# Performance work log

Hardware: AMD Instinct MI355X
Metric: run time of the kernel (lower is better)

## Reference

```python
import jax, jax.numpy as jnp
import numpy as np

NUM_HEADS = 12
ROPE_THETA = 10000.0


def _rope_cos_sin(n, hd, dtype):
    inv_freq = 1.0 / (ROPE_THETA ** (np.arange(0, hd, 2, dtype=np.float64) / hd))
    freqs = np.outer(np.arange(n, dtype=np.float64), inv_freq)  # (N, hd/2)
    emb = np.concatenate([freqs, freqs], axis=-1)               # (N, hd)
    return jnp.asarray(np.cos(emb), dtype), jnp.asarray(np.sin(emb), dtype)


def _apply_rope(t, cos, sin):
    # t: (B, H, N, hd); rotate-half convention
    half = t.shape[-1] // 2
    t1, t2 = t[..., :half], t[..., half:]
    rot = jnp.concatenate([-t2, t1], axis=-1)
    return t * cos + rot * sin


def setup_inputs() -> dict:
    key = jax.random.key(0)
    k1, k2, k3 = jax.random.split(key, 3)
    B, N, C = 8, 1024, 768
    x = jax.random.normal(k1, (B, N, C), dtype=jnp.float32)
    w_qkv = jax.random.normal(k2, (C, 3 * C), dtype=jnp.float32) * 0.02
    w_proj = jax.random.normal(k3, (C, C), dtype=jnp.float32) * 0.02
    b_proj = jnp.zeros((C,), dtype=jnp.float32)
    return {"x": x, "w_qkv": w_qkv, "w_proj": w_proj, "b_proj": b_proj}


def reference(x, w_qkv, w_proj, b_proj):
    B, N, C = x.shape
    H = NUM_HEADS
    hd = C // H
    scale = hd ** -0.5
    # qkv: (B,N,3C) -> (B,N,3,H,hd) -> (B,H,3,N,hd)
    qkv = (x @ w_qkv).reshape(B, N, 3, H, hd).transpose(0, 3, 2, 1, 4)
    q, k, v = qkv[:, :, 0], qkv[:, :, 1], qkv[:, :, 2]  # each (B,H,N,hd)
    cos, sin = _rope_cos_sin(N, hd, x.dtype)
    q = _apply_rope(q, cos, sin)
    k = _apply_rope(k, cos, sin)
    attn = jax.nn.softmax(jnp.einsum("bhqd,bhkd->bhqk", q, k) * scale, axis=-1)
    out = jnp.einsum("bhqk,bhkd->bhqd", attn, v)  # (B,H,N,hd)
    out = out.transpose(0, 2, 1, 3).reshape(B, N, C)
    return out @ w_proj + b_proj
```

## Files before the change

kernel.cpp:

```cpp
#include <hip/hip_runtime.h>

typedef unsigned short ushort_t;
typedef __bf16 bf16x8 __attribute__((ext_vector_type(8)));
typedef float f32x4 __attribute__((ext_vector_type(4)));
typedef unsigned short u16x8 __attribute__((ext_vector_type(8)));
typedef unsigned int u32x2 __attribute__((ext_vector_type(2)));

#define MFMA16(a, b, c) __builtin_amdgcn_mfma_f32_16x16x32_bf16((a), (b), (c), 0, 0, 0)

#define SEQ 1024
#define NHEAD 12
#define HD 64
#define CDIM 768
#define TS 6291456
#define QSCALE 0.1803368801111204f

__device__ __forceinline__ ushort_t f2bf(float f) {
  __bf16 b = (__bf16)f;
  return __builtin_bit_cast(ushort_t, b);
}
__device__ __forceinline__ unsigned pk2(float lo, float hi) {
  return (unsigned)f2bf(lo) | ((unsigned)f2bf(hi) << 16);
}

typedef __attribute__((address_space(1))) void gvoid_t;
typedef __attribute__((address_space(3))) void lvoid_t;
__device__ __forceinline__ void async16(const ushort_t* g, ushort_t* l) {
  __builtin_amdgcn_global_load_lds((gvoid_t*)g, (lvoid_t*)l, 16, 0, 0);
}

__device__ __forceinline__ void transpose_body(const float* __restrict__ in,
                                               ushort_t* __restrict__ out,
                                               int R, int C, int bxi, int byi,
                                               float (*tile)[33]) {
  int bx = bxi * 32, by = byi * 32;
  int tx = threadIdx.x & 31, ty = threadIdx.x >> 5;
#pragma unroll
  for (int i = ty; i < 32; i += 8) {
    int r = by + i, c = bx + tx;
    if (r < R && c < C) tile[i][tx] = in[(size_t)r * C + c];
  }
  __syncthreads();
#pragma unroll
  for (int i = ty; i < 32; i += 8) {
    int r = bx + i, c = by + tx;
    if (r < C && c < R) out[(size_t)r * R + c] = f2bf(tile[tx][i]);
  }
}

__global__ void __launch_bounds__(256) prep_all(const float* __restrict__ x,
                                                const float* __restrict__ w_qkv,
                                                const float* __restrict__ w_proj,
                                                ushort_t* __restrict__ xb,
                                                ushort_t* __restrict__ wqkvT,
                                                ushort_t* __restrict__ wprojT,
                                                float* __restrict__ tab) {
  __shared__ float tile[32][33];
  const int bid = blockIdx.x;
  if (bid < 3072) {
    int i = (bid * 256 + threadIdx.x) * 8;
    float4 a = *(const float4*)(x + i);
    float4 b = *(const float4*)(x + i + 4);
    u16x8 r;
    r[0] = f2bf(a.x); r[1] = f2bf(a.y); r[2] = f2bf(a.z); r[3] = f2bf(a.w);
    r[4] = f2bf(b.x); r[5] = f2bf(b.y); r[6] = f2bf(b.z); r[7] = f2bf(b.w);
    *(u16x8*)(xb + i) = r;
  } else if (bid < 3072 + 1728) {
    int t = bid - 3072;
    transpose_body(w_qkv, wqkvT, 768, 2304, t % 72, t / 72, tile);
  } else if (bid < 3072 + 1728 + 576) {
    int t = bid - (3072 + 1728);
    transpose_body(w_proj, wprojT, 768, 768, t % 24, t / 24, tile);
  } else {
    int g = (bid - 5376) * 256 + threadIdx.x;
    int n = g >> 5, j = g & 31;
    double invf = pow(10000.0, -((double)(2 * j)) / 64.0);
    double fr = (double)n * invf;
    tab[g * 2]     = (float)cos(fr);
    tab[g * 2 + 1] = (float)sin(fr);
  }
}

__device__ __forceinline__ void gemm_bt_core(const ushort_t* __restrict__ A,
                                             const ushort_t* __restrict__ Bt,
                                             int K, int bm, int bn,
                                             ushort_t (*ldsA)[4096],
                                             ushort_t (*ldsB)[4096],
                                             f32x4 acc[4][4]) {
  const int tid = threadIdx.x;
  const int lane = tid & 63, wid = tid >> 6;
  const int wm = (wid >> 1) * 64, wn = (wid & 1) * 64;
  const int fr = lane & 15, fq = lane >> 4;
#pragma unroll
  for (int i = 0; i < 4; ++i)
#pragma unroll
    for (int j = 0; j < 4; ++j) acc[i][j] = (f32x4){0.f, 0.f, 0.f, 0.f};

  const int srow = tid >> 2;
  const int scol = (tid & 3) * 8;
  const size_t aOff = (size_t)(bm + srow) * K + scol;
  const size_t bOff = (size_t)(bn + srow) * K + scol;
  const int nIter = K >> 6;

  for (int kt = 0; kt < nIter; ++kt) {
    const int k0 = kt * 64;
#pragma unroll
    for (int h = 0; h < 2; ++h) {
      async16(A + aOff + k0 + h * 32, ldsA[h] + tid * 8);
      async16(A + aOff + (size_t)64 * K + k0 + h * 32, ldsA[h] + 2048 + tid * 8);
      async16(Bt + bOff + k0 + h * 32, ldsB[h] + tid * 8);
      async16(Bt + bOff + (size_t)64 * K + k0 + h * 32, ldsB[h] + 2048 + tid * 8);
    }
    __syncthreads();
#pragma unroll
    for (int ks = 0; ks < 2; ++ks) {
      bf16x8 aF[4], bF[4];
#pragma unroll
      for (int i = 0; i < 4; ++i)
        aF[i] = *(const bf16x8*)(ldsA[ks] + (wm + i * 16 + fr) * 32 + fq * 8);
#pragma unroll
      for (int j = 0; j < 4; ++j)
        bF[j] = *(const bf16x8*)(ldsB[ks] + (wn + j * 16 + fr) * 32 + fq * 8);
#pragma unroll
      for (int i = 0; i < 4; ++i)
#pragma unroll
        for (int j = 0; j < 4; ++j) acc[i][j] = MFMA16(aF[i], bF[j], acc[i][j]);
    }
    __syncthreads();
  }
}

__global__ void __launch_bounds__(256) gemm_qkv(const ushort_t* __restrict__ A,
                                                const ushort_t* __restrict__ Bt,
                                                const float* __restrict__ tab,
                                                ushort_t* __restrict__ qkv) {
  __shared__ __attribute__((aligned(16))) ushort_t ldsA[2][4096];
  __shared__ __attribute__((aligned(16))) ushort_t ldsB[2][4096];
  f32x4 acc[4][4];
  const int f = blockIdx.x;
  const int xcd = f & 7, r = f >> 3;
  const int bm = (xcd * 8 + (r & 7)) * 128;
  const int bn = (r >> 3) * 128;
  gemm_bt_core(A, Bt, CDIM, bm, bn, ldsA, ldsB, acc);
  const int lane = threadIdx.x & 63, wid = threadIdx.x >> 6;
  const int wm = (wid >> 1) * 64, wn = (wid & 1) * 64;
  const int fr = lane & 15, fq = lane >> 4;
  const int tensor = bn / 768;

  if (tensor < 2) {
    ushort_t* dstT = qkv + (size_t)tensor * TS;
    const float qs = (tensor == 0) ? QSCALE : 1.0f;
#pragma unroll
    for (int i = 0; i < 4; ++i) {
#pragma unroll
      for (int jp = 0; jp < 2; ++jp) {
        const int col = bn + wn + jp * 16 + fr;
        const int rem = col - tensor * 768;
        const int h = rem >> 6;
        const int d2 = rem & 31;
#pragma unroll
        for (int rr = 0; rr < 4; ++rr) {
          const int row = bm + wm + i * 16 + fq * 4 + rr;
          const int b = row >> 10, n = row & 1023;
          const float2 cs = ((const float2*)tab)[n * 32 + d2];
          const float av = acc[i][jp][rr], bv = acc[i][jp + 2][rr];
          const float o1 = (av * cs.x - bv * cs.y) * qs;
          const float o2 = (bv * cs.x + av * cs.y) * qs;
          ushort_t* dst = dstT + ((size_t)(b * NHEAD + h) * SEQ + n) * HD + d2;
          dst[0]  = f2bf(o1);
          dst[32] = f2bf(o2);
        }
      }
    }
  } else {
    ushort_t* vt = qkv + 2 * (size_t)TS;
#pragma unroll
    for (int i = 0; i < 4; ++i) {
      const int row0 = bm + wm + i * 16 + fq * 4;
      const int b = row0 >> 10, n0 = row0 & 1023;
#pragma unroll
      for (int j = 0; j < 4; ++j) {
        const int col = bn + wn + j * 16 + fr;
        const int rem = col - 1536;
        const int h = rem >> 6, d = rem & 63;
        u32x2 pk;
        pk[0] = pk2(acc[i][j][0], acc[i][j][1]);
        pk[1] = pk2(acc[i][j][2], acc[i][j][3]);
        *(u32x2*)(vt + ((size_t)(b * NHEAD + h) * HD + d) * SEQ + n0) = pk;
      }
    }
  }
}

__global__ void __launch_bounds__(256) gemm_proj(const ushort_t* __restrict__ A,
                                                 const ushort_t* __restrict__ Bt,
                                                 const float* __restrict__ bias,
                                                 float* __restrict__ Cout) {
  __shared__ __attribute__((aligned(16))) ushort_t ldsA[2][4096];
  __shared__ __attribute__((aligned(16))) ushort_t ldsB[2][4096];
  f32x4 acc[4][4];
  const int f = blockIdx.x;
  const int xcd = f & 7, r = f >> 3;
  const int bm = (xcd * 8 + (r & 7)) * 128;
  const int bn = (r >> 3) * 128;
  gemm_bt_core(A, Bt, CDIM, bm, bn, ldsA, ldsB, acc);
  const int lane = threadIdx.x & 63, wid = threadIdx.x >> 6;
  const int wm = (wid >> 1) * 64, wn = (wid & 1) * 64;
  const int fr = lane & 15, fq = lane >> 4;
#pragma unroll
  for (int i = 0; i < 4; ++i) {
#pragma unroll
    for (int j = 0; j < 4; ++j) {
      const int col = bn + wn + j * 16 + fr;
      const float bv = bias[col];
#pragma unroll
      for (int rr = 0; rr < 4; ++rr) {
        const int row = bm + wm + i * 16 + fq * 4 + rr;
        Cout[(size_t)row * CDIM + col] = acc[i][j][rr] + bv;
      }
    }
  }
}

__global__ void __launch_bounds__(256, 3) attn_fused(const ushort_t* __restrict__ Qb,
                                                     const ushort_t* __restrict__ Kb,
                                                     const ushort_t* __restrict__ VTb,
                                                     ushort_t* __restrict__ Ob) {
  __shared__ __attribute__((aligned(16))) ushort_t ldsK[2][2][2048];
  __shared__ __attribute__((aligned(16))) ushort_t ldsV[2][2][2048];
  __shared__ __attribute__((aligned(16))) ushort_t Pl[4][32 * 72];

  const int tid = threadIdx.x, lane = tid & 63, wid = tid >> 6;
  const int fr = lane & 15, fq = lane >> 4;

  const int f = blockIdx.x;
  const int xp = f & 7, rest = f >> 3;
  const int g = rest % 12, qb = rest / 12;
  const int head = g * 8 + xp;
  const int q0 = qb * 128;

  const ushort_t* Qh  = Qb  + (size_t)head * (SEQ * HD);
  const ushort_t* Kh  = Kb  + (size_t)head * (SEQ * HD);
  const ushort_t* VTh = VTb + (size_t)head * (HD * SEQ);

  bf16x8 qF[2][2];
#pragma unroll
  for (int qt = 0; qt < 2; ++qt) {
    const int qrow = q0 + wid * 32 + qt * 16 + fr;
    qF[qt][0] = *(const bf16x8*)(Qh + (size_t)qrow * HD + fq * 8);
    qF[qt][1] = *(const bf16x8*)(Qh + (size_t)qrow * HD + 32 + fq * 8);
  }

  f32x4 ot[2][4];
#pragma unroll
  for (int qt = 0; qt < 2; ++qt)
#pragma unroll
    for (int dt = 0; dt < 4; ++dt) ot[qt][dt] = (f32x4){0.f, 0.f, 0.f, 0.f};
  float lsum[2] = {0.f, 0.f};

  const int srow = tid >> 2;
  const int sc = (tid & 3) * 8;

#define STAGE(buf, kt)                                                          \
  {                                                                             \
    const ushort_t* ksrc = Kh + (size_t)((kt) * 64 + srow) * HD + sc;           \
    async16(ksrc,      &ldsK[buf][0][tid * 8]);                                 \
    async16(ksrc + 32, &ldsK[buf][1][tid * 8]);                                 \
    const ushort_t* vsrc = VTh + (size_t)srow * SEQ + (kt) * 64 + sc;           \
    async16(vsrc,      &ldsV[buf][0][tid * 8]);                                 \
    async16(vsrc + 32, &ldsV[buf][1][tid * 8]);                                 \
  }

  STAGE(0, 0);
  __syncthreads();

  for (int kt = 0; kt < 16; ++kt) {
    const int cur = kt & 1;
    if (kt < 15) STAGE(cur ^ 1, kt + 1);

    bf16x8 kf[4][2];
#pragma unroll
    for (int t = 0; t < 4; ++t)
#pragma unroll
      for (int ks = 0; ks < 2; ++ks)
        kf[t][ks] = *(const bf16x8*)&ldsK[cur][ks][(t * 16 + fr) * 32 + fq * 8];

    f32x4 st[2][4];
#pragma unroll
    for (int qt = 0; qt < 2; ++qt)
#pragma unroll
      for (int t = 0; t < 4; ++t) {
        f32x4 s = (f32x4){0.f, 0.f, 0.f, 0.f};
        s = MFMA16(kf[t][0], qF[qt][0], s);
        s = MFMA16(kf[t][1], qF[qt][1], s);
        st[qt][t] = s;
      }

    bf16x8 vf[4][2];
#pragma unroll
    for (int dt = 0; dt < 4; ++dt)
#pragma unroll
      for (int ks = 0; ks < 2; ++ks)
        vf[dt][ks] = *(const bf16x8*)&ldsV[cur][ks][(dt * 16 + fr) * 32 + fq * 8];

#pragma unroll
    for (int qt = 0; qt < 2; ++qt) {
      ushort_t* Pw = &Pl[wid][(qt * 16 + fr) * 72];
      float ls = lsum[qt];
#pragma unroll
      for (int t = 0; t < 4; ++t) {
        const float e0 = exp2f(st[qt][t][0]);
        const float e1 = exp2f(st[qt][t][1]);
        const float e2 = exp2f(st[qt][t][2]);
        const float e3 = exp2f(st[qt][t][3]);
        ls += (e0 + e1) + (e2 + e3);
        u32x2 pk;
        pk[0] = pk2(e0, e1);
        pk[1] = pk2(e2, e3);
        *(u32x2*)(Pw + t * 16 + fq * 4) = pk;
      }
      lsum[qt] = ls;
      bf16x8 pf0 = *(const bf16x8*)(Pw + fq * 8);
      bf16x8 pf1 = *(const bf16x8*)(Pw + 32 + fq * 8);
#pragma unroll
      for (int dt = 0; dt < 4; ++dt) {
        ot[qt][dt] = MFMA16(vf[dt][0], pf0, ot[qt][dt]);
        ot[qt][dt] = MFMA16(vf[dt][1], pf1, ot[qt][dt]);
      }
    }
    __syncthreads();
  }

  const int b = head / NHEAD, h = head - b * NHEAD;
#pragma unroll
  for (int qt = 0; qt < 2; ++qt) {
    float l = lsum[qt];
    l += __shfl_xor(l, 16);
    l += __shfl_xor(l, 32);
    const float inv = 1.0f / l;
    const int qrow = q0 + wid * 32 + qt * 16 + fr;
    ushort_t* obase = Ob + ((size_t)(b * SEQ + qrow)) * CDIM + h * HD;
#pragma unroll
    for (int dt = 0; dt < 4; ++dt) {
      u32x2 pk;
      pk[0] = pk2(ot[qt][dt][0] * inv, ot[qt][dt][1] * inv);
      pk[1] = pk2(ot[qt][dt][2] * inv, ot[qt][dt][3] * inv);
      *(u32x2*)(obase + dt * 16 + fq * 4) = pk;
    }
  }
}

extern "C" void kernel_launch(void* const* d_in, const int* in_sizes, int n_in,
                              void* d_out, int out_size, void* d_ws, size_t ws_size,
                              hipStream_t stream) {
  const float* x      = (const float*)d_in[0];
  const float* w_qkv  = (const float*)d_in[1];
  const float* w_proj = (const float*)d_in[2];
  const float* b_proj = (const float*)d_in[3];
  float* out = (float*)d_out;
  char* ws = (char*)d_ws;

  ushort_t* xb     = (ushort_t*)(ws + 0);
  ushort_t* wqkvT  = (ushort_t*)(ws + 12582912);
  ushort_t* wprojT = (ushort_t*)(ws + 16121856);
  ushort_t* qkv    = (ushort_t*)(ws + 17301504);
  float*    tab    = (float*)  (ws + 55050240);
  ushort_t* oattn  = (ushort_t*)(ws + 55312384);

  prep_all<<<5504, 256, 0, stream>>>(x, w_qkv, w_proj, xb, wqkvT, wprojT, tab);
  gemm_qkv<<<1152, 256, 0, stream>>>(xb, wqkvT, tab, qkv);
  attn_fused<<<768, 256, 0, stream>>>(qkv, qkv + TS, qkv + 2 * (size_t)TS, oattn);
  gemm_proj<<<384, 256, 0, stream>>>(oattn, wprojT, b_proj, out);
}
```

Before: 210.9 us.

## Switch attention to 32x32x16 MFMA with register-resident P and swizzled LDS

Rewrites the attention kernel to use 32x32x16 bf16 MFMA tiles instead of 16x16x32, so each wave handles its 32 query rows with one accumulator per output half. The probability matrix is now rearranged into the B-operand layout with cross-half-wave shuffles instead of a round trip through a per-wave LDS buffer. K/V tiles are stored in LDS with an XOR-style swizzle to avoid bank conflicts. The aim is to cut LDS traffic and instruction count per tile. The cost is larger accumulator registers, and the occupancy hint in launch bounds is dropped.

```diff
diff --git a/kernel.cpp b/kernel.cpp
--- a/kernel.cpp
+++ b/kernel.cpp
@@ -3,10 +3,13 @@
 typedef unsigned short ushort_t;
 typedef __bf16 bf16x8 __attribute__((ext_vector_type(8)));
 typedef float f32x4 __attribute__((ext_vector_type(4)));
+typedef float f32x16 __attribute__((ext_vector_type(16)));
 typedef unsigned short u16x8 __attribute__((ext_vector_type(8)));
 typedef unsigned int u32x2 __attribute__((ext_vector_type(2)));
+typedef unsigned int u32x4 __attribute__((ext_vector_type(4)));
 
 #define MFMA16(a, b, c) __builtin_amdgcn_mfma_f32_16x16x32_bf16((a), (b), (c), 0, 0, 0)
+#define MFMA32(a, b, c) __builtin_amdgcn_mfma_f32_32x32x16_bf16((a), (b), (c), 0, 0, 0)
 
 #define SEQ 1024
 #define NHEAD 12
@@ -222,16 +225,15 @@
   }
 }
 
-__global__ void __launch_bounds__(256, 3) attn_fused(const ushort_t* __restrict__ Qb,
-                                                     const ushort_t* __restrict__ Kb,
-                                                     const ushort_t* __restrict__ VTb,
-                                                     ushort_t* __restrict__ Ob) {
-  __shared__ __attribute__((aligned(16))) ushort_t ldsK[2][2][2048];
-  __shared__ __attribute__((aligned(16))) ushort_t ldsV[2][2][2048];
-  __shared__ __attribute__((aligned(16))) ushort_t Pl[4][32 * 72];
+__global__ void __launch_bounds__(256) attn_fused(const ushort_t* __restrict__ Qb,
+                                                  const ushort_t* __restrict__ Kb,
+                                                  const ushort_t* __restrict__ VTb,
+                                                  ushort_t* __restrict__ Ob) {
+  __shared__ __attribute__((aligned(16))) ushort_t ldsK[2][4096];
+  __shared__ __attribute__((aligned(16))) ushort_t ldsV[2][4096];
 
   const int tid = threadIdx.x, lane = tid & 63, wid = tid >> 6;
-  const int fr = lane & 15, fq = lane >> 4;
+  const int l31 = lane & 31, h = lane >> 5;
 
   const int f = blockIdx.x;
   const int xp = f & 7, rest = f >> 3;
@@ -243,109 +245,108 @@
   const ushort_t* Kh  = Kb  + (size_t)head * (SEQ * HD);
   const ushort_t* VTh = VTb + (size_t)head * (HD * SEQ);
 
-  bf16x8 qF[2][2];
-#pragma unroll
-  for (int qt = 0; qt < 2; ++qt) {
-    const int qrow = q0 + wid * 32 + qt * 16 + fr;
-    qF[qt][0] = *(const bf16x8*)(Qh + (size_t)qrow * HD + fq * 8);
-    qF[qt][1] = *(const bf16x8*)(Qh + (size_t)qrow * HD + 32 + fq * 8);
-  }
-
-  f32x4 ot[2][4];
-#pragma unroll
-  for (int qt = 0; qt < 2; ++qt)
-#pragma unroll
-    for (int dt = 0; dt < 4; ++dt) ot[qt][dt] = (f32x4){0.f, 0.f, 0.f, 0.f};
-  float lsum[2] = {0.f, 0.f};
-
-  const int srow = tid >> 2;
-  const int sc = (tid & 3) * 8;
-
-#define STAGE(buf, kt)                                                          \
+  const int qrow = q0 + wid * 32 + l31;
+  bf16x8 qF[4];
+#pragma unroll
+  for (int dk = 0; dk < 4; ++dk)
+    qF[dk] = *(const bf16x8*)(Qh + (size_t)qrow * HD + dk * 16 + 8 * h);
+
+  f32x16 ot[2];
+#pragma unroll
+  for (int dt = 0; dt < 2; ++dt)
+#pragma unroll
+    for (int i = 0; i < 16; ++i) ot[dt][i] = 0.f;
+  float lsum = 0.f;
+
+  const int s0 = tid, s1 = tid + 256;
+  const int r0 = s0 >> 3, c0 = ((s0 & 7) - r0) & 7;
+  const int r1 = s1 >> 3, c1 = ((s1 & 7) - r1) & 7;
+
+#define ASTAGE(buf, kt)                                                         \
   {                                                                             \
-    const ushort_t* ksrc = Kh + (size_t)((kt) * 64 + srow) * HD + sc;           \
-    async16(ksrc,      &ldsK[buf][0][tid * 8]);                                 \
-    async16(ksrc + 32, &ldsK[buf][1][tid * 8]);                                 \
-    const ushort_t* vsrc = VTh + (size_t)srow * SEQ + (kt) * 64 + sc;           \
-    async16(vsrc,      &ldsV[buf][0][tid * 8]);                                 \
-    async16(vsrc + 32, &ldsV[buf][1][tid * 8]);                                 \
-  }
-
-  STAGE(0, 0);
+    async16(Kh + (size_t)((kt) * 64 + r0) * HD + c0 * 8, &ldsK[buf][s0 * 8]);   \
+    async16(Kh + (size_t)((kt) * 64 + r1) * HD + c1 * 8, &ldsK[buf][s1 * 8]);   \
+    async16(VTh + (size_t)r0 * SEQ + (kt) * 64 + c0 * 8, &ldsV[buf][s0 * 8]);   \
+    async16(VTh + (size_t)r1 * SEQ + (kt) * 64 + c1 * 8, &ldsV[buf][s1 * 8]);   \
+  }
+
+  ASTAGE(0, 0);
   __syncthreads();
 
   for (int kt = 0; kt < 16; ++kt) {
     const int cur = kt & 1;
-    if (kt < 15) STAGE(cur ^ 1, kt + 1);
-
-    bf16x8 kf[4][2];
-#pragma unroll
-    for (int t = 0; t < 4; ++t)
-#pragma unroll
-      for (int ks = 0; ks < 2; ++ks)
-        kf[t][ks] = *(const bf16x8*)&ldsK[cur][ks][(t * 16 + fr) * 32 + fq * 8];
-
-    f32x4 st[2][4];
-#pragma unroll
-    for (int qt = 0; qt < 2; ++qt)
-#pragma unroll
-      for (int t = 0; t < 4; ++t) {
-        f32x4 s = (f32x4){0.f, 0.f, 0.f, 0.f};
-        s = MFMA16(kf[t][0], qF[qt][0], s);
-        s = MFMA16(kf[t][1], qF[qt][1], s);
-        st[qt][t] = s;
-      }
-
-    bf16x8 vf[4][2];
-#pragma unroll
-    for (int dt = 0; dt < 4; ++dt)
-#pragma unroll
-      for (int ks = 0; ks < 2; ++ks)
-        vf[dt][ks] = *(const bf16x8*)&ldsV[cur][ks][(dt * 16 + fr) * 32 + fq * 8];
-
-#pragma unroll
-    for (int qt = 0; qt < 2; ++qt) {
-      ushort_t* Pw = &Pl[wid][(qt * 16 + fr) * 72];
-      float ls = lsum[qt];
-#pragma unroll
-      for (int t = 0; t < 4; ++t) {
-        const float e0 = exp2f(st[qt][t][0]);
-        const float e1 = exp2f(st[qt][t][1]);
-        const float e2 = exp2f(st[qt][t][2]);
-        const float e3 = exp2f(st[qt][t][3]);
-        ls += (e0 + e1) + (e2 + e3);
-        u32x2 pk;
-        pk[0] = pk2(e0, e1);
-        pk[1] = pk2(e2, e3);
-        *(u32x2*)(Pw + t * 16 + fq * 4) = pk;
-      }
-      lsum[qt] = ls;
-      bf16x8 pf0 = *(const bf16x8*)(Pw + fq * 8);
-      bf16x8 pf1 = *(const bf16x8*)(Pw + 32 + fq * 8);
-#pragma unroll
-      for (int dt = 0; dt < 4; ++dt) {
-        ot[qt][dt] = MFMA16(vf[dt][0], pf0, ot[qt][dt]);
-        ot[qt][dt] = MFMA16(vf[dt][1], pf1, ot[qt][dt]);
+    if (kt < 15) ASTAGE(cur ^ 1, kt + 1);
+
+    f32x16 st[2];
+#pragma unroll
+    for (int ks = 0; ks < 2; ++ks) {
+      f32x16 s;
+#pragma unroll
+      for (int i = 0; i < 16; ++i) s[i] = 0.f;
+      const int kr = ks * 32 + l31;
+#pragma unroll
+      for (int dk = 0; dk < 4; ++dk) {
+        const int sw = (dk * 2 + h + kr) & 7;
+        bf16x8 kf = *(const bf16x8*)&ldsK[cur][(kr * 8 + sw) * 8];
+        s = MFMA32(kf, qF[dk], s);
+      }
+      st[ks] = s;
+    }
+
+    unsigned pk[2][8];
+#pragma unroll
+    for (int ks = 0; ks < 2; ++ks) {
+      float ls = 0.f;
+#pragma unroll
+      for (int m = 0; m < 8; ++m) {
+        const float e0 = exp2f(st[ks][2 * m]);
+        const float e1 = exp2f(st[ks][2 * m + 1]);
+        ls += e0 + e1;
+        pk[ks][m] = pk2(e0, e1);
+      }
+      lsum += ls;
+    }
+
+#pragma unroll
+    for (int kc = 0; kc < 4; ++kc) {
+      const int ks = kc >> 1, mb = (kc & 1) * 4;
+      const unsigned sA = h ? pk[ks][mb + 2] : pk[ks][mb + 0];
+      const unsigned sB = h ? pk[ks][mb + 3] : pk[ks][mb + 1];
+      const unsigned uA = h ? pk[ks][mb + 0] : pk[ks][mb + 2];
+      const unsigned uB = h ? pk[ks][mb + 1] : pk[ks][mb + 3];
+      const unsigned xA = (unsigned)__shfl_xor((int)uA, 32);
+      const unsigned xB = (unsigned)__shfl_xor((int)uB, 32);
+      u32x4 bi;
+      bi[0] = h ? xA : sA;
+      bi[1] = h ? xB : sB;
+      bi[2] = h ? sA : xA;
+      bi[3] = h ? sB : xB;
+      const bf16x8 pf = __builtin_bit_cast(bf16x8, bi);
+#pragma unroll
+      for (int dt = 0; dt < 2; ++dt) {
+        const int dr = dt * 32 + l31;
+        const int sw = (kc * 2 + h + dr) & 7;
+        bf16x8 vf = *(const bf16x8*)&ldsV[cur][(dr * 8 + sw) * 8];
+        ot[dt] = MFMA32(vf, pf, ot[dt]);
       }
     }
     __syncthreads();
   }
-
-  const int b = head / NHEAD, h = head - b * NHEAD;
-#pragma unroll
-  for (int qt = 0; qt < 2; ++qt) {
-    float l = lsum[qt];
-    l += __shfl_xor(l, 16);
-    l += __shfl_xor(l, 32);
-    const float inv = 1.0f / l;
-    const int qrow = q0 + wid * 32 + qt * 16 + fr;
-    ushort_t* obase = Ob + ((size_t)(b * SEQ + qrow)) * CDIM + h * HD;
-#pragma unroll
-    for (int dt = 0; dt < 4; ++dt) {
-      u32x2 pk;
-      pk[0] = pk2(ot[qt][dt][0] * inv, ot[qt][dt][1] * inv);
-      pk[1] = pk2(ot[qt][dt][2] * inv, ot[qt][dt][3] * inv);
-      *(u32x2*)(obase + dt * 16 + fq * 4) = pk;
+#undef ASTAGE
+
+  lsum += __shfl_xor(lsum, 32);
+  const float inv = 1.0f / lsum;
+  const int b = head / NHEAD, hh = head - b * NHEAD;
+  ushort_t* obase = Ob + ((size_t)(b * SEQ + qrow)) * CDIM + hh * HD;
+#pragma unroll
+  for (int dt = 0; dt < 2; ++dt) {
+#pragma unroll
+    for (int r2 = 0; r2 < 4; ++r2) {
+      const int d = dt * 32 + 8 * r2 + 4 * h;
+      u32x2 w;
+      w[0] = pk2(ot[dt][4 * r2 + 0] * inv, ot[dt][4 * r2 + 1] * inv);
+      w[1] = pk2(ot[dt][4 * r2 + 2] * inv, ot[dt][4 * r2 + 3] * inv);
+      *(u32x2*)(obase + d) = w;
     }
   }
 }
```

New measurement: 206.0 us. 1.02x faster.
